# Performance work log

Measured on AMD Instinct MI355X. Metric: run time of the kernel, lower is better.

The kernel has to match this reference:

```python
import jax, jax.numpy as jnp
import numpy as np

N, D = 16384, 128

def setup_inputs() -> dict:
    key = jax.random.key(0)
    k1, k2 = jax.random.split(key)
    x = jax.random.normal(k1, (N, D), dtype=jnp.float32)
    adj = jax.random.randint(k2, (N, N), 0, 2, dtype=jnp.int32)
    return {"x": x, "adj": adj}

def reference(x, adj):
    # out[i] = x[i] + sum_{j: adj[i,j]==1} x[j]  ==  (adj + I) @ x
    a = adj.astype(x.dtype)
    return x + jnp.matmul(a, x)  # [N, D]
```

## Files before the change

kernel.cpp:

```cpp
#include <hip/hip_runtime.h>
#include <hip/hip_bf16.h>

#define GN 16384
#define GD 128
#define KSPLIT 4
#define KBLK (GN / KSPLIT)
#define PHK 128
#define NPH (KBLK / PHK)
#define NSTEP (PHK / 32)
#define BUF_SHORTS (GD * PHK)
#define OUT_ELEMS (GN * GD)

typedef __attribute__((ext_vector_type(8))) short short8;
typedef __attribute__((ext_vector_type(4))) float floatx4;
typedef __attribute__((ext_vector_type(4))) int intx4;

static __device__ __forceinline__ unsigned short f32_to_bf16(float f) {
  unsigned u = __builtin_bit_cast(unsigned, f);
  unsigned r = u + 0x7FFFu + ((u >> 16) & 1u);
  return (unsigned short)(r >> 16);
}

__global__ __launch_bounds__(256) void prep_kernel(const float* __restrict__ x,
                                                   unsigned short* __restrict__ xT) {
  __shared__ unsigned short t[GD][66];
  const int tid = threadIdx.x;
  const int j0 = blockIdx.x * 64;
  for (int i = tid; i < 64 * GD; i += 256) {
    int j = i >> 7, d = i & (GD - 1);
    t[d][j] = f32_to_bf16(x[(size_t)(j0 + j) * GD + d]);
  }
  __syncthreads();
  for (int i = tid; i < GD * 32; i += 256) {
    int d = i >> 5, jp = i & 31;
    unsigned lo = t[d][2 * jp], hi = t[d][2 * jp + 1];
    *reinterpret_cast<unsigned*>(xT + (size_t)d * GN + j0 + 2 * jp) = lo | (hi << 16);
  }
}

__global__ __launch_bounds__(512, 4) void gemm_kernel(const int* __restrict__ adj,
                                                      const unsigned short* __restrict__ xT,
                                                      float* __restrict__ partials) {
  __shared__ unsigned short bbuf[2][BUF_SHORTS];
  const int tid = threadIdx.x;
  const int wave = tid >> 6;
  const int lane = tid & 63;
  const int q = lane >> 4;
  const int m = lane & 15;
  const int rbase = blockIdx.x * 128 + wave * 16;
  const int ks = blockIdx.y;
  const int kbase = ks * KBLK;

  const unsigned short* gptr[4];
  unsigned short* lptr[4];
#pragma unroll
  for (int p = 0; p < 4; ++p) {
    int s = tid + 512 * p;
    int n = s >> 4;
    int gsrc = (s & 15) ^ (n & 7);
    gptr[p] = xT + (size_t)n * GN + kbase + gsrc * 8;
    lptr[p] = &bbuf[0][0] + (size_t)s * 8;
  }

#define STAGE(bufsel, koff)                                                             \
  do {                                                                                  \
    _Pragma("unroll") for (int p = 0; p < 4; ++p) {                                     \
      __builtin_amdgcn_global_load_lds(                                                 \
          (const __attribute__((address_space(1))) unsigned int*)(gptr[p] + (koff)),    \
          (__attribute__((address_space(3))) unsigned int*)(lptr[p] +                   \
                                                           (bufsel) * BUF_SHORTS),      \
          16, 0, 0);                                                                    \
    }                                                                                   \
  } while (0)

  const int* a0 = adj + (size_t)(rbase + m) * GN + kbase + q * 8;

  floatx4 acc[8];
#pragma unroll
  for (int c = 0; c < 8; ++c) acc[c] = (floatx4){0.f, 0.f, 0.f, 0.f};

  STAGE(0, 0);
  intx4 cadj[8];
#pragma unroll
  for (int u = 0; u < 8; ++u)
    cadj[u] = *(const intx4*)(a0 + (u >> 1) * 32 + (u & 1) * 4);

  int buf = 0;
  for (int ph = 0; ph < NPH; ++ph) {
    __syncthreads();
    intx4 nadj[8];
    if (ph + 1 < NPH) {
      STAGE(buf ^ 1, (ph + 1) * PHK);
      const int* an = a0 + (ph + 1) * PHK;
#pragma unroll
      for (int u = 0; u < 8; ++u)
        nadj[u] = *(const intx4*)(an + (u >> 1) * 32 + (u & 1) * 4);
    }

#pragma unroll
    for (int st = 0; st < NSTEP; ++st) {
      short8 bf[8];
      const unsigned short* bb = &bbuf[buf][0] + (((st * 4 + q) ^ (m & 7)) * 8);
#pragma unroll
      for (int cc = 0; cc < 8; ++cc)
        bf[cc] = *(const short8*)(bb + (cc * 16 + m) * PHK);

      const intx4 r0 = cadj[2 * st], r1 = cadj[2 * st + 1];
      intx4 pk;
      pk.x = (r0.x | (r0.y << 16)) * 0x3F80;
      pk.y = (r0.z | (r0.w << 16)) * 0x3F80;
      pk.z = (r1.x | (r1.y << 16)) * 0x3F80;
      pk.w = (r1.z | (r1.w << 16)) * 0x3F80;
      const short8 af = __builtin_bit_cast(short8, pk);

#pragma unroll
      for (int cc = 0; cc < 8; ++cc)
        acc[cc] = __builtin_amdgcn_mfma_f32_16x16x32_bf16(af, bf[cc], acc[cc], 0, 0, 0);
    }

#pragma unroll
    for (int u = 0; u < 8; ++u) cadj[u] = nadj[u];
    buf ^= 1;
  }

  float* pp = partials + (size_t)ks * OUT_ELEMS + (size_t)rbase * GD;
#pragma unroll
  for (int cc = 0; cc < 8; ++cc)
#pragma unroll
    for (int r = 0; r < 4; ++r)
      pp[(size_t)(q * 4 + r) * GD + cc * 16 + m] = acc[cc][r];
}

__global__ __launch_bounds__(256) void reduce_kernel(const float* __restrict__ x,
                                                     const float* __restrict__ partials,
                                                     float* __restrict__ out) {
  size_t i = ((size_t)blockIdx.x * 256 + threadIdx.x) * 4;
  floatx4 v = *(const floatx4*)(x + i);
  v += *(const floatx4*)(partials + 0 * (size_t)OUT_ELEMS + i);
  v += *(const floatx4*)(partials + 1 * (size_t)OUT_ELEMS + i);
  v += *(const floatx4*)(partials + 2 * (size_t)OUT_ELEMS + i);
  v += *(const floatx4*)(partials + 3 * (size_t)OUT_ELEMS + i);
  *(floatx4*)(out + i) = v;
}

extern "C" void kernel_launch(void* const* d_in, const int* in_sizes, int n_in,
                              void* d_out, int out_size, void* d_ws, size_t ws_size,
                              hipStream_t stream) {
  const float* x = (const float*)d_in[0];
  const int* adj = (const int*)d_in[1];
  float* out = (float*)d_out;
  unsigned short* xT = (unsigned short*)d_ws;
  float* partials = (float*)((char*)d_ws + (size_t)GN * GD * 2);

  prep_kernel<<<GN / 64, 256, 0, stream>>>(x, xT);
  gemm_kernel<<<dim3(GN / 128, KSPLIT), 512, 0, stream>>>(adj, xT, partials);
  reduce_kernel<<<OUT_ELEMS / 4 / 256, 256, 0, stream>>>(x, partials, out);
}
```

Measured before the change: 1.350 ms.

## Pack adjacency into bitmask in a separate pass before the MFMA GEMM

Adds a pack kernel that compresses the int32 0/1 adjacency matrix into 32-bit bitmasks, one bit per entry. The GEMM then loads one 16-byte word per lane per phase instead of eight, and expands the bits into bf16 ones with integer arithmetic. This reduces register pressure and load latency in the MFMA loop. The cost is a separate streaming pass over the full adjacency matrix plus a 32 MB workspace write.

```diff
diff --git a/kernel.cpp b/kernel.cpp
--- a/kernel.cpp
+++ b/kernel.cpp
@@ -10,10 +10,12 @@
 #define NSTEP (PHK / 32)
 #define BUF_SHORTS (GD * PHK)
 #define OUT_ELEMS (GN * GD)
+#define GNW (GN / 32)
 
 typedef __attribute__((ext_vector_type(8))) short short8;
 typedef __attribute__((ext_vector_type(4))) float floatx4;
 typedef __attribute__((ext_vector_type(4))) int intx4;
+typedef __attribute__((ext_vector_type(4))) unsigned uintx4;
 
 static __device__ __forceinline__ unsigned short f32_to_bf16(float f) {
   unsigned u = __builtin_bit_cast(unsigned, f);
@@ -38,7 +40,25 @@
   }
 }
 
-__global__ __launch_bounds__(512, 4) void gemm_kernel(const int* __restrict__ adj,
+__global__ __launch_bounds__(256) void pack_kernel(const int* __restrict__ adj,
+                                                   unsigned* __restrict__ ubits) {
+  const size_t total = (size_t)GN * GNW;
+  size_t idx = (size_t)blockIdx.x * 256 + threadIdx.x;
+  const size_t stride = (size_t)gridDim.x * 256;
+  for (; idx < total; idx += stride) {
+    const int* p = adj + idx * 32;
+    unsigned res = 0;
+#pragma unroll
+    for (int j = 0; j < 8; ++j) {
+      intx4 r = *(const intx4*)(p + j * 4);
+      unsigned n = (unsigned)(r.x | (r.y << 1) | (r.z << 2) | (r.w << 3));
+      res |= n << (4 * j);
+    }
+    ubits[idx] = res;
+  }
+}
+
+__global__ __launch_bounds__(512, 4) void gemm_kernel(const unsigned* __restrict__ ubits,
                                                       const unsigned short* __restrict__ xT,
                                                       float* __restrict__ partials) {
   __shared__ unsigned short bbuf[2][BUF_SHORTS];
@@ -73,28 +93,22 @@
     }                                                                                   \
   } while (0)
 
-  const int* a0 = adj + (size_t)(rbase + m) * GN + kbase + q * 8;
+  const unsigned* ub = ubits + (size_t)(rbase + m) * GNW + (kbase >> 5);
 
   floatx4 acc[8];
 #pragma unroll
   for (int c = 0; c < 8; ++c) acc[c] = (floatx4){0.f, 0.f, 0.f, 0.f};
 
   STAGE(0, 0);
-  intx4 cadj[8];
-#pragma unroll
-  for (int u = 0; u < 8; ++u)
-    cadj[u] = *(const intx4*)(a0 + (u >> 1) * 32 + (u & 1) * 4);
+  uintx4 cw = *(const uintx4*)(ub);
 
   int buf = 0;
   for (int ph = 0; ph < NPH; ++ph) {
     __syncthreads();
-    intx4 nadj[8];
+    uintx4 nw;
     if (ph + 1 < NPH) {
       STAGE(buf ^ 1, (ph + 1) * PHK);
-      const int* an = a0 + (ph + 1) * PHK;
-#pragma unroll
-      for (int u = 0; u < 8; ++u)
-        nadj[u] = *(const intx4*)(an + (u >> 1) * 32 + (u & 1) * 4);
+      nw = *(const uintx4*)(ub + (size_t)(ph + 1) * 4);
     }
 
 #pragma unroll
@@ -105,12 +119,14 @@
       for (int cc = 0; cc < 8; ++cc)
         bf[cc] = *(const short8*)(bb + (cc * 16 + m) * PHK);
 
-      const intx4 r0 = cadj[2 * st], r1 = cadj[2 * st + 1];
+      const unsigned w = cw[st];
+      const unsigned b = (w >> (q * 8)) & 0xFFu;
       intx4 pk;
-      pk.x = (r0.x | (r0.y << 16)) * 0x3F80;
-      pk.y = (r0.z | (r0.w << 16)) * 0x3F80;
-      pk.z = (r1.x | (r1.y << 16)) * 0x3F80;
-      pk.w = (r1.z | (r1.w << 16)) * 0x3F80;
+#pragma unroll
+      for (int j = 0; j < 4; ++j) {
+        unsigned t = (b >> (2 * j)) & 3u;
+        pk[j] = (int)(((t * 0x8001u) & 0x10001u) * 0x3F80u);
+      }
       const short8 af = __builtin_bit_cast(short8, pk);
 
 #pragma unroll
@@ -118,8 +134,7 @@
         acc[cc] = __builtin_amdgcn_mfma_f32_16x16x32_bf16(af, bf[cc], acc[cc], 0, 0, 0);
     }
 
-#pragma unroll
-    for (int u = 0; u < 8; ++u) cadj[u] = nadj[u];
+    cw = nw;
     buf ^= 1;
   }
 
@@ -151,8 +166,11 @@
   float* out = (float*)d_out;
   unsigned short* xT = (unsigned short*)d_ws;
   float* partials = (float*)((char*)d_ws + (size_t)GN * GD * 2);
+  unsigned* ubits = (unsigned*)((char*)d_ws + (size_t)GN * GD * 2 +
+                                (size_t)KSPLIT * OUT_ELEMS * 4);
 
   prep_kernel<<<GN / 64, 256, 0, stream>>>(x, xT);
-  gemm_kernel<<<dim3(GN / 128, KSPLIT), 512, 0, stream>>>(adj, xT, partials);
+  pack_kernel<<<2048, 256, 0, stream>>>(adj, ubits);
+  gemm_kernel<<<dim3(GN / 128, KSPLIT), 512, 0, stream>>>(ubits, xT, partials);
   reduce_kernel<<<OUT_ELEMS / 4 / 256, 256, 0, stream>>>(x, partials, out);
 }
```

Result: slower. 1.431 ms (+6.0%).

## Drop LDS staging of B; load xT fragments directly from global per wave

Applied to the files above, without the earlier changes.

Removes the shared-memory double buffer and block-wide syncs for the xT operand. Each wave now reads its B fragments straight from global memory (relying on L2/L1 reuse) and keeps a 4-step register prefetch ring for adjacency rows. Blocks shrink to 256 threads (4 waves, 64 rows), doubling the grid. This trades LDS traffic and barriers for redundant global/L2 reads of xT across waves.

```diff
diff --git a/kernel.cpp b/kernel.cpp
--- a/kernel.cpp
+++ b/kernel.cpp
@@ -5,10 +5,7 @@
 #define GD 128
 #define KSPLIT 4
 #define KBLK (GN / KSPLIT)
-#define PHK 128
-#define NPH (KBLK / PHK)
-#define NSTEP (PHK / 32)
-#define BUF_SHORTS (GD * PHK)
+#define STEPS (KBLK / 32)
 #define OUT_ELEMS (GN * GD)
 
 typedef __attribute__((ext_vector_type(8))) short short8;
@@ -38,74 +35,42 @@
   }
 }
 
-__global__ __launch_bounds__(512, 4) void gemm_kernel(const int* __restrict__ adj,
+__global__ __launch_bounds__(256, 4) void gemm_kernel(const int* __restrict__ adj,
                                                       const unsigned short* __restrict__ xT,
                                                       float* __restrict__ partials) {
-  __shared__ unsigned short bbuf[2][BUF_SHORTS];
   const int tid = threadIdx.x;
   const int wave = tid >> 6;
   const int lane = tid & 63;
   const int q = lane >> 4;
   const int m = lane & 15;
-  const int rbase = blockIdx.x * 128 + wave * 16;
+  const int tile = blockIdx.x * 4 + wave;
+  const int rbase = tile * 16;
   const int ks = blockIdx.y;
   const int kbase = ks * KBLK;
 
-  const unsigned short* gptr[4];
-  unsigned short* lptr[4];
-#pragma unroll
-  for (int p = 0; p < 4; ++p) {
-    int s = tid + 512 * p;
-    int n = s >> 4;
-    int gsrc = (s & 15) ^ (n & 7);
-    gptr[p] = xT + (size_t)n * GN + kbase + gsrc * 8;
-    lptr[p] = &bbuf[0][0] + (size_t)s * 8;
-  }
-
-#define STAGE(bufsel, koff)                                                             \
-  do {                                                                                  \
-    _Pragma("unroll") for (int p = 0; p < 4; ++p) {                                     \
-      __builtin_amdgcn_global_load_lds(                                                 \
-          (const __attribute__((address_space(1))) unsigned int*)(gptr[p] + (koff)),    \
-          (__attribute__((address_space(3))) unsigned int*)(lptr[p] +                   \
-                                                           (bufsel) * BUF_SHORTS),      \
-          16, 0, 0);                                                                    \
-    }                                                                                   \
-  } while (0)
-
-  const int* a0 = adj + (size_t)(rbase + m) * GN + kbase + q * 8;
+  const int* arow = adj + (size_t)(rbase + m) * GN + kbase + q * 8;
+  const unsigned short* brow = xT + (size_t)m * GN + kbase + q * 8;
 
   floatx4 acc[8];
 #pragma unroll
   for (int c = 0; c < 8; ++c) acc[c] = (floatx4){0.f, 0.f, 0.f, 0.f};
 
-  STAGE(0, 0);
-  intx4 cadj[8];
+  intx4 ra[4], rb[4];
 #pragma unroll
-  for (int u = 0; u < 8; ++u)
-    cadj[u] = *(const intx4*)(a0 + (u >> 1) * 32 + (u & 1) * 4);
+  for (int j = 0; j < 4; ++j) {
+    ra[j] = *(const intx4*)(arow + j * 32);
+    rb[j] = *(const intx4*)(arow + j * 32 + 4);
+  }
 
-  int buf = 0;
-  for (int ph = 0; ph < NPH; ++ph) {
-    __syncthreads();
-    intx4 nadj[8];
-    if (ph + 1 < NPH) {
-      STAGE(buf ^ 1, (ph + 1) * PHK);
-      const int* an = a0 + (ph + 1) * PHK;
+  for (int ch = 0; ch < STEPS; ch += 4) {
 #pragma unroll
-      for (int u = 0; u < 8; ++u)
-        nadj[u] = *(const intx4*)(an + (u >> 1) * 32 + (u & 1) * 4);
-    }
+    for (int j = 0; j < 4; ++j) {
+      const int s = ch + j;
+      const intx4 r0 = ra[j], r1 = rb[j];
+      const int sn = (s + 4) & (STEPS - 1);
+      ra[j] = *(const intx4*)(arow + sn * 32);
+      rb[j] = *(const intx4*)(arow + sn * 32 + 4);
 
-#pragma unroll
-    for (int st = 0; st < NSTEP; ++st) {
-      short8 bf[8];
-      const unsigned short* bb = &bbuf[buf][0] + (((st * 4 + q) ^ (m & 7)) * 8);
-#pragma unroll
-      for (int cc = 0; cc < 8; ++cc)
-        bf[cc] = *(const short8*)(bb + (cc * 16 + m) * PHK);
-
-      const intx4 r0 = cadj[2 * st], r1 = cadj[2 * st + 1];
       intx4 pk;
       pk.x = (r0.x | (r0.y << 16)) * 0x3F80;
       pk.y = (r0.z | (r0.w << 16)) * 0x3F80;
@@ -113,14 +78,15 @@
       pk.w = (r1.z | (r1.w << 16)) * 0x3F80;
       const short8 af = __builtin_bit_cast(short8, pk);
 
+      short8 bf[8];
+#pragma unroll
+      for (int cc = 0; cc < 8; ++cc)
+        bf[cc] = *(const short8*)(brow + (size_t)cc * (16 * GN) + s * 32);
+
 #pragma unroll
       for (int cc = 0; cc < 8; ++cc)
         acc[cc] = __builtin_amdgcn_mfma_f32_16x16x32_bf16(af, bf[cc], acc[cc], 0, 0, 0);
     }
-
-#pragma unroll
-    for (int u = 0; u < 8; ++u) cadj[u] = nadj[u];
-    buf ^= 1;
   }
 
   float* pp = partials + (size_t)ks * OUT_ELEMS + (size_t)rbase * GD;
@@ -153,6 +119,6 @@
   float* partials = (float*)((char*)d_ws + (size_t)GN * GD * 2);
 
   prep_kernel<<<GN / 64, 256, 0, stream>>>(x, xT);
-  gemm_kernel<<<dim3(GN / 128, KSPLIT), 512, 0, stream>>>(adj, xT, partials);
+  gemm_kernel<<<dim3(GN / 64, KSPLIT), 256, 0, stream>>>(adj, xT, partials);
   reduce_kernel<<<OUT_ELEMS / 4 / 256, 256, 0, stream>>>(x, partials, out);
 }
```

Result: slower. 1.712 ms (+26.9%).
